# Kernel tuning notes

Measured on AMD Instinct MI355X. Metric: run time of the kernel, lower is better.

## Reference

```python
import jax, jax.numpy as jnp
import numpy as np

N_NODES = 10000
IN_DIM = 128
H1 = 32
H2 = 16
N_EDGES = 640000


def gcn_conv(x, W, b, row, col, n):
    """PyG-style GCNConv: add self-loops, symmetric deg^{-1/2} norm, linear, scatter-add."""
    loop = jnp.arange(n, dtype=row.dtype)
    r = jnp.concatenate([row, loop])
    c = jnp.concatenate([col, loop])
    deg = jax.ops.segment_sum(jnp.ones(r.shape[0], dtype=x.dtype), c, num_segments=n)
    dinv = jnp.where(deg > 0, jax.lax.rsqrt(deg), 0.0)
    norm = dinv[r] * dinv[c]                      # (E+N,)
    h = x @ W                                     # (N, out)
    msg = h[r] * norm[:, None]                    # gather + scale
    out = jax.ops.segment_sum(msg, c, num_segments=n)  # scatter-add
    return out + b


def setup_inputs() -> dict:
    key = jax.random.key(0)
    k1, k2, k3, k4, k5, k6 = jax.random.split(key, 6)
    x = jax.random.normal(k1, (N_NODES, IN_DIM), dtype=jnp.float32)
    edge_index = jax.random.randint(k2, (2, N_EDGES), 0, N_NODES, dtype=jnp.int64)
    # glorot-ish init for weights, zeros for bias (PyG defaults)
    W1 = jax.random.normal(k3, (IN_DIM, H1), dtype=jnp.float32) / np.sqrt(IN_DIM)
    b1 = jnp.zeros((H1,), dtype=jnp.float32)
    W2 = jax.random.normal(k4, (H1, H2), dtype=jnp.float32) / np.sqrt(H1)
    b2 = jnp.zeros((H2,), dtype=jnp.float32)
    return {"x": x, "edge_index": edge_index, "W1": W1, "b1": b1, "W2": W2, "b2": b2}


def reference(x, edge_index, W1, b1, W2, b2):
    row, col = edge_index[0], edge_index[1]
    n = x.shape[0]
    h = jax.nn.relu(gcn_conv(x, W1, b1, row, col, n))  # (N, H1)
    z = gcn_conv(h, W2, b2, row, col, n)               # (N, H2)
    logits = z @ z.T                                   # (N, N) dot-product decode
    return logits
```

## Files before the change

### kernel.cpp

```cpp
#include <hip/hip_runtime.h>

#define IN_DIM 128
#define H1 32
#define H2 16
#define PAD 160

#define XNODES 8
__global__ void k_fill_mm1(const int* __restrict__ row, const int* __restrict__ col,
                           int* __restrict__ deg, int* __restrict__ csrpad, int E,
                           const float* __restrict__ x, const float* __restrict__ W1,
                           float* __restrict__ hout, int N, int fillBlocks) {
    __shared__ float Ws[IN_DIM * H1];
    __shared__ float xs[XNODES][IN_DIM];
    if ((int)blockIdx.x < fillBlocks) {
        int e = blockIdx.x * blockDim.x + threadIdx.x;
        if (e < E) {
            int c = col[e];
            int pos = atomicAdd(&deg[c], 1);
            csrpad[(long)c * PAD + pos] = row[e];
        }
        return;
    }
    int t = threadIdx.x;
    int i0 = ((int)blockIdx.x - fillBlocks) * XNODES;
    const float4* W4 = reinterpret_cast<const float4*>(W1);
    float4* Ws4 = reinterpret_cast<float4*>(Ws);
#pragma unroll
    for (int i = t; i < IN_DIM * H1 / 4; i += 256) Ws4[i] = W4[i];
    const float4* xg = reinterpret_cast<const float4*>(x + (long)i0 * IN_DIM);
    float4* xs4 = reinterpret_cast<float4*>(xs);
    xs4[t] = xg[t];
    __syncthreads();
    int n = t >> 5, d = t & 31;
    float acc = 0.f;
#pragma unroll 8
    for (int k = 0; k < IN_DIM; ++k) acc = fmaf(xs[n][k], Ws[k * H1 + d], acc);
    int i = i0 + n;
    if (i < N) hout[(long)i * H1 + d] = acc;
}

__global__ void k_prep(const int* __restrict__ deg, float* __restrict__ dinv,
                       float* __restrict__ h, int N) {
    int i = blockIdx.x * blockDim.x + threadIdx.x;
    if (i >= N) return;
    float di = rsqrtf((float)deg[i] + 1.0f);
    dinv[i] = di;
    float4* hp = reinterpret_cast<float4*>(h + (long)i * H1);
#pragma unroll
    for (int q = 0; q < H1 / 4; ++q) {
        float4 v = hp[q];
        v.x *= di; v.y *= di; v.z *= di; v.w *= di;
        hp[q] = v;
    }
}

__global__ void k_g1mm2(const int* __restrict__ deg, const int* __restrict__ csrpad,
                        const float* __restrict__ dinv, const float* __restrict__ hp,
                        const float* __restrict__ b1, const float* __restrict__ W2,
                        float* __restrict__ h2p, int N) {
    __shared__ float W2s[H1 * H2];
    __shared__ float h1s[4][H1];
    int t = threadIdx.x;
    for (int i = t; i < H1 * H2; i += blockDim.x) W2s[i] = W2[i];
    __syncthreads();
    int wv = t >> 6;
    int lane = t & 63;
    int c = blockIdx.x * 4 + wv;
    bool active = (c < N);
    int cc = active ? c : (N - 1);
    constexpr int C4 = H1 / 4;
    constexpr int SUB = 64 / C4;
    int sub = lane / C4, d4 = lane % C4;
    int cnt = deg[cc];
    const int* bin = csrpad + (long)cc * PAD;
    const float4* hp4 = reinterpret_cast<const float4*>(hp);

    float4 A0 = make_float4(0.f, 0.f, 0.f, 0.f), A1 = A0, A2 = A0, A3 = A0;
    int k = sub;
    for (; k + 3 * SUB < cnt; k += 4 * SUB) {
        int s0 = bin[k];
        int s1 = bin[k + SUB];
        int s2 = bin[k + 2 * SUB];
        int s3 = bin[k + 3 * SUB];
        float4 v0 = hp4[(long)s0 * C4 + d4];
        float4 v1 = hp4[(long)s1 * C4 + d4];
        float4 v2 = hp4[(long)s2 * C4 + d4];
        float4 v3 = hp4[(long)s3 * C4 + d4];
        A0.x += v0.x; A0.y += v0.y; A0.z += v0.z; A0.w += v0.w;
        A1.x += v1.x; A1.y += v1.y; A1.z += v1.z; A1.w += v1.w;
        A2.x += v2.x; A2.y += v2.y; A2.z += v2.z; A2.w += v2.w;
        A3.x += v3.x; A3.y += v3.y; A3.z += v3.z; A3.w += v3.w;
    }
    for (; k < cnt; k += SUB) {
        float4 v = hp4[(long)bin[k] * C4 + d4];
        A0.x += v.x; A0.y += v.y; A0.z += v.z; A0.w += v.w;
    }
    float4 acc;
    acc.x = (A0.x + A1.x) + (A2.x + A3.x);
    acc.y = (A0.y + A1.y) + (A2.y + A3.y);
    acc.z = (A0.z + A1.z) + (A2.z + A3.z);
    acc.w = (A0.w + A1.w) + (A2.w + A3.w);
#pragma unroll
    for (int off = C4; off < 64; off <<= 1) {
        acc.x += __shfl_xor(acc.x, off, 64);
        acc.y += __shfl_xor(acc.y, off, 64);
        acc.z += __shfl_xor(acc.z, off, 64);
        acc.w += __shfl_xor(acc.w, off, 64);
    }
    if (lane < C4) {
        float di = dinv[cc];
        float4 self = hp4[(long)cc * C4 + d4];
        float4 bv = reinterpret_cast<const float4*>(b1)[d4];
        float4 v;
        v.x = fmaxf(fmaf(di, acc.x + self.x, bv.x), 0.f);
        v.y = fmaxf(fmaf(di, acc.y + self.y, bv.y), 0.f);
        v.z = fmaxf(fmaf(di, acc.z + self.z, bv.z), 0.f);
        v.w = fmaxf(fmaf(di, acc.w + self.w, bv.w), 0.f);
        reinterpret_cast<float4*>(h1s[wv])[d4] = v;
    }
    __syncthreads();
    if (active && lane < H2) {
        float z = 0.f;
#pragma unroll
        for (int kk = 0; kk < H1; ++kk) z = fmaf(h1s[wv][kk], W2s[kk * H2 + lane], z);
        h2p[(long)c * H2 + lane] = z * dinv[c];
    }
}

template <int D, bool RELU>
__global__ void k_gather(const int* __restrict__ deg, const int* __restrict__ csrpad,
                         const float* __restrict__ dinv, const float* __restrict__ hp,
                         const float* __restrict__ bias, float* __restrict__ out, int N) {
    constexpr int C4  = D / 4;
    constexpr int SUB = 64 / C4;
    int c = blockIdx.x * (blockDim.x >> 6) + (threadIdx.x >> 6);
    if (c >= N) return;
    int lane = threadIdx.x & 63;
    int sub = lane / C4, d4 = lane % C4;
    int cnt = deg[c];
    const int* bin = csrpad + (long)c * PAD;
    const float4* hp4 = reinterpret_cast<const float4*>(hp);

    float4 A0 = make_float4(0.f, 0.f, 0.f, 0.f), A1 = A0, A2 = A0, A3 = A0;
    int k = sub;
    for (; k + 3 * SUB < cnt; k += 4 * SUB) {
        int s0 = bin[k];
        int s1 = bin[k + SUB];
        int s2 = bin[k + 2 * SUB];
        int s3 = bin[k + 3 * SUB];
        float4 v0 = hp4[(long)s0 * C4 + d4];
        float4 v1 = hp4[(long)s1 * C4 + d4];
        float4 v2 = hp4[(long)s2 * C4 + d4];
        float4 v3 = hp4[(long)s3 * C4 + d4];
        A0.x += v0.x; A0.y += v0.y; A0.z += v0.z; A0.w += v0.w;
        A1.x += v1.x; A1.y += v1.y; A1.z += v1.z; A1.w += v1.w;
        A2.x += v2.x; A2.y += v2.y; A2.z += v2.z; A2.w += v2.w;
        A3.x += v3.x; A3.y += v3.y; A3.z += v3.z; A3.w += v3.w;
    }
    for (; k < cnt; k += SUB) {
        float4 v = hp4[(long)bin[k] * C4 + d4];
        A0.x += v.x; A0.y += v.y; A0.z += v.z; A0.w += v.w;
    }
    float4 acc;
    acc.x = (A0.x + A1.x) + (A2.x + A3.x);
    acc.y = (A0.y + A1.y) + (A2.y + A3.y);
    acc.z = (A0.z + A1.z) + (A2.z + A3.z);
    acc.w = (A0.w + A1.w) + (A2.w + A3.w);
#pragma unroll
    for (int off = C4; off < 64; off <<= 1) {
        acc.x += __shfl_xor(acc.x, off, 64);
        acc.y += __shfl_xor(acc.y, off, 64);
        acc.z += __shfl_xor(acc.z, off, 64);
        acc.w += __shfl_xor(acc.w, off, 64);
    }
    if (lane < C4) {
        float di = dinv[c];
        float4 self = hp4[(long)c * C4 + d4];
        float4 bv = reinterpret_cast<const float4*>(bias)[d4];
        float4 v;
        v.x = fmaf(di, acc.x + self.x, bv.x);
        v.y = fmaf(di, acc.y + self.y, bv.y);
        v.z = fmaf(di, acc.z + self.z, bv.z);
        v.w = fmaf(di, acc.w + self.w, bv.w);
        if (RELU) {
            v.x = fmaxf(v.x, 0.f); v.y = fmaxf(v.y, 0.f);
            v.z = fmaxf(v.z, 0.f); v.w = fmaxf(v.w, 0.f);
        }
        reinterpret_cast<float4*>(out + (long)c * D)[d4] = v;
    }
}


__global__ void k_count(const int* __restrict__ col, int* __restrict__ deg, int E) {
    int e = blockIdx.x * blockDim.x + threadIdx.x;
    if (e < E) atomicAdd(&deg[col[e]], 1);
}

template <int KD, int OD, bool SCALE>
__global__ void k_mm(const float* __restrict__ xin, const float* __restrict__ W,
                     const float* __restrict__ dinv, float* __restrict__ hout, int N) {
    __shared__ float Ws[KD * OD];
    for (int t = threadIdx.x; t < KD * OD; t += blockDim.x) Ws[t] = W[t];
    __syncthreads();
    int idx = blockIdx.x * blockDim.x + threadIdx.x;
    int i = idx / OD, d = idx % OD;
    if (i >= N) return;
    const float4* xr = reinterpret_cast<const float4*>(xin + (long)i * KD);
    float acc = 0.f;
#pragma unroll
    for (int k4 = 0; k4 < KD / 4; ++k4) {
        float4 xv = xr[k4];
        acc = fmaf(xv.x, Ws[(4 * k4 + 0) * OD + d], acc);
        acc = fmaf(xv.y, Ws[(4 * k4 + 1) * OD + d], acc);
        acc = fmaf(xv.z, Ws[(4 * k4 + 2) * OD + d], acc);
        acc = fmaf(xv.w, Ws[(4 * k4 + 3) * OD + d], acc);
    }
    hout[idx] = SCALE ? acc * dinv[i] : acc;
}

__global__ void k_dinv_i(const int* __restrict__ deg, float* __restrict__ dinv, int N) {
    int i = blockIdx.x * blockDim.x + threadIdx.x;
    if (i < N) dinv[i] = rsqrtf((float)deg[i] + 1.0f);
}

template <int D>
__global__ void k_scatter(const int* __restrict__ row, const int* __restrict__ col,
                          const float* __restrict__ dinv, const float* __restrict__ hin,
                          float* __restrict__ agg, int E) {
    int idx = blockIdx.x * blockDim.x + threadIdx.x;
    int e = idx / D, d = idx % D;
    if (e >= E) return;
    int r = row[e], c = col[e];
    float nrm = dinv[r] * dinv[c];
    atomicAdd(&agg[(long)c * D + d], hin[(long)r * D + d] * nrm);
}

template <int D, bool RELU>
__global__ void k_finish(const float* __restrict__ hproj, const float* __restrict__ dinv,
                         const float* __restrict__ bias, float* __restrict__ agg, int N) {
    int idx = blockIdx.x * blockDim.x + threadIdx.x;
    if (idx >= N * D) return;
    int i = idx / D, d = idx % D;
    float di = dinv[i];
    float v = agg[idx] + hproj[idx] * di * di + bias[d];
    agg[idx] = RELU ? fmaxf(v, 0.f) : v;
}

#define DT 128

__global__ __launch_bounds__(512, 8)
void k_decode(const float* __restrict__ z, float* __restrict__ out, int N) {
    __shared__ float ziT[16][DT];
    __shared__ float zjT[16][DT];
    int bi = blockIdx.y * DT, bj = blockIdx.x * DT;
    int t = threadIdx.x;

    {
        int r = (t >> 1) & 127;
        int gi = (t < 256 ? bi : bj) + r;
        int half = t & 1;
        float4 v0 = make_float4(0.f, 0.f, 0.f, 0.f), v1 = v0;
        if (gi < N) {
            const float4* zp = reinterpret_cast<const float4*>(z + (long)gi * 16);
            v0 = zp[half * 2];
            v1 = zp[half * 2 + 1];
        }
        float vals[8] = {v0.x, v0.y, v0.z, v0.w, v1.x, v1.y, v1.z, v1.w};
        float (*dst)[DT] = (t < 256) ? ziT : zjT;
        int k0 = half * 8;
#pragma unroll
        for (int k = 0; k < 8; ++k) dst[k0 + k][r] = vals[k];
    }
    __syncthreads();

    int tx = t & 15, ty = t >> 4;
    float acc[4][8] = {};
#pragma unroll 4
    for (int k = 0; k < 16; ++k) {
        float a[4], b[8];
        float4 a0 = *reinterpret_cast<const float4*>(&ziT[k][ty * 4]);
        float4 b0 = *reinterpret_cast<const float4*>(&zjT[k][tx * 4]);
        float4 b1 = *reinterpret_cast<const float4*>(&zjT[k][64 + tx * 4]);
        a[0]=a0.x; a[1]=a0.y; a[2]=a0.z; a[3]=a0.w;
        b[0]=b0.x; b[1]=b0.y; b[2]=b0.z; b[3]=b0.w;
        b[4]=b1.x; b[5]=b1.y; b[6]=b1.z; b[7]=b1.w;
#pragma unroll
        for (int u = 0; u < 4; ++u)
#pragma unroll
            for (int v = 0; v < 8; ++v)
                acc[u][v] = fmaf(a[u], b[v], acc[u][v]);
    }

#pragma unroll
    for (int u = 0; u < 4; ++u) {
        int gi = bi + ty * 4 + u;
        if (gi >= N) continue;
        int gj0 = bj + tx * 4;
        int gj1 = bj + 64 + tx * 4;
        long rowb = (long)gi * N;
        if (gj0 + 3 < N) {
            *reinterpret_cast<float4*>(&out[rowb + gj0]) =
                make_float4(acc[u][0], acc[u][1], acc[u][2], acc[u][3]);
        } else {
            for (int v2 = 0; v2 < 4; ++v2)
                if (gj0 + v2 < N) out[rowb + gj0 + v2] = acc[u][v2];
        }
        if (gj1 + 3 < N) {
            *reinterpret_cast<float4*>(&out[rowb + gj1]) =
                make_float4(acc[u][4], acc[u][5], acc[u][6], acc[u][7]);
        } else {
            for (int v2 = 0; v2 < 4; ++v2)
                if (gj1 + v2 < N) out[rowb + gj1 + v2] = acc[u][4 + v2];
        }
    }
}


extern "C" void kernel_launch(void* const* d_in, const int* in_sizes, int n_in,
                              void* d_out, int out_size, void* d_ws, size_t ws_size,
                              hipStream_t stream) {
    const float* x  = (const float*)d_in[0];
    const int*   ei = (const int*)d_in[1];
    const float* W1 = (const float*)d_in[2];
    const float* b1 = (const float*)d_in[3];
    const float* W2 = (const float*)d_in[4];
    const float* b2 = (const float*)d_in[5];
    float* out = (float*)d_out;

    const int N = in_sizes[0] / IN_DIM;
    const int E = in_sizes[1] / 2;
    const int* row = ei;
    const int* col = ei + E;

    const long SZ_DEG = (N + 15) & ~15L;
    const long SZ_BIN = (long)N * PAD;
    const long SZ_DI  = SZ_DEG;
    const long need = SZ_DEG + SZ_BIN + SZ_DI
                    + (long)N * H1 + 2L * N * H2;

    if (ws_size >= (size_t)need * 4) {
        int*   deg    = (int*)d_ws;
        int*   csrpad = deg + SZ_DEG;
        float* dinv   = (float*)(csrpad + SZ_BIN);
        float* h      = dinv + SZ_DI;
        float* h2p    = h + (long)N * H1;
        float* zz     = h2p + (long)N * H2;

        hipMemsetAsync(deg, 0, (size_t)N * sizeof(int), stream);

        int fillBlocks = (E + 255) / 256;
        int mmBlocks   = (N + XNODES - 1) / XNODES;
        k_fill_mm1<<<fillBlocks + mmBlocks, 256, 0, stream>>>(
            row, col, deg, csrpad, E, x, W1, h, N, fillBlocks);

        k_prep<<<(N + 255) / 256, 256, 0, stream>>>(deg, dinv, h, N);

        k_g1mm2<<<(N + 3) / 4, 256, 0, stream>>>(deg, csrpad, dinv, h, b1, W2, h2p, N);
        k_gather<H2, false><<<(N + 3) / 4, 256, 0, stream>>>(deg, csrpad, dinv, h2p, b2, zz, N);

        dim3 dgrid((N + DT - 1) / DT, (N + DT - 1) / DT);
        k_decode<<<dgrid, 512, 0, stream>>>(zz, out, N);
    } else {
        int*   deg  = (int*)d_ws;
        float* dinv = (float*)(deg + SZ_DEG);
        float* h    = dinv + SZ_DI;
        float* h1   = h + (long)N * H1;
        float* h2   = h1 + (long)N * H1;
        float* zz   = h2 + (long)N * H2;

        hipMemsetAsync(deg, 0, (size_t)N * sizeof(int), stream);
        hipMemsetAsync(h1, 0, (size_t)N * H1 * sizeof(float), stream);
        hipMemsetAsync(zz, 0, (size_t)N * H2 * sizeof(float), stream);

        k_count<<<(E + 255) / 256, 256, 0, stream>>>(col, deg, E);
        k_dinv_i<<<(N + 255) / 256, 256, 0, stream>>>(deg, dinv, N);

        k_mm<IN_DIM, H1, false><<<((long)N * H1 + 255) / 256, 256, 0, stream>>>(x, W1, dinv, h, N);
        k_scatter<H1><<<((long)E * H1 + 255) / 256, 256, 0, stream>>>(row, col, dinv, h, h1, E);
        k_finish<H1, true><<<((long)N * H1 + 255) / 256, 256, 0, stream>>>(h, dinv, b1, h1, N);

        k_mm<H1, H2, false><<<((long)N * H2 + 255) / 256, 256, 0, stream>>>(h1, W2, dinv, h2, N);
        k_scatter<H2><<<((long)E * H2 + 255) / 256, 256, 0, stream>>>(row, col, dinv, h2, zz, E);
        k_finish<H2, false><<<((long)N * H2 + 255) / 256, 256, 0, stream>>>(h2, dinv, b2, zz, N);

        dim3 dgrid((N + DT - 1) / DT, (N + DT - 1) / DT);
        k_decode<<<dgrid, 512, 0, stream>>>(zz, out, N);
    }
}
```

Before: 170.5 us.

## Fuse GCN pre-decode stages into one cooperative persistent kernel with grid syncs

Replaces the memset and the four pre-decode kernels (fill+mm1, prep, gather+mm2, gather) with one cooperative kernel of 512 persistent blocks. The stages are separated by grid.sync() calls. The aim is to remove per-kernel launch and drain overhead in the small-graph GCN stages. The cost is grid-wide barriers and lower parallelism per stage, since only 512 blocks run. The non-cooperative fallback path is also removed.

```diff
diff --git a/kernel.cpp b/kernel.cpp
--- a/kernel.cpp
+++ b/kernel.cpp
@@ -1,11 +1,201 @@
 #include <hip/hip_runtime.h>
+#include <hip/hip_cooperative_groups.h>
+namespace cg = cooperative_groups;
 
 #define IN_DIM 128
 #define H1 32
 #define H2 16
 #define PAD 160
-
 #define XNODES 8
+#define MGRID 512
+
+__global__ __launch_bounds__(256, 4) void k_mega(
+    const int* __restrict__ row, const int* __restrict__ col,
+    int* __restrict__ deg, int* __restrict__ csrpad,
+    const float* __restrict__ x, const float* __restrict__ W1,
+    const float* __restrict__ b1, const float* __restrict__ W2,
+    const float* __restrict__ b2, float* __restrict__ dinv,
+    float* __restrict__ h, float* __restrict__ h2p, float* __restrict__ zz,
+    int N, int E) {
+    cg::grid_group grid = cg::this_grid();
+    __shared__ float Ws[IN_DIM * H1];
+    __shared__ float xs[XNODES][IN_DIM];
+    __shared__ float h1s[4][H1];
+    int t = threadIdx.x;
+    int nth = (int)(gridDim.x * blockDim.x);
+    int gtid = (int)(blockIdx.x * blockDim.x) + t;
+
+    for (int i = gtid; i < N; i += nth) deg[i] = 0;
+    grid.sync();
+
+    for (int e = gtid; e < E; e += nth) {
+        int c = col[e];
+        int pos = atomicAdd(&deg[c], 1);
+        csrpad[(long)c * PAD + pos] = row[e];
+    }
+    {
+        const float4* W4 = reinterpret_cast<const float4*>(W1);
+        float4* Ws4 = reinterpret_cast<float4*>(Ws);
+        for (int i = t; i < IN_DIM * H1 / 4; i += 256) Ws4[i] = W4[i];
+    }
+    int ngroups = (N + XNODES - 1) / XNODES;
+    for (int g = (int)blockIdx.x; g < ngroups; g += (int)gridDim.x) {
+        __syncthreads();
+        int i0 = g * XNODES;
+        int gi = i0 + (t >> 5);
+        float4 xv = make_float4(0.f, 0.f, 0.f, 0.f);
+        if (gi < N) xv = reinterpret_cast<const float4*>(x)[(long)i0 * 32 + t];
+        reinterpret_cast<float4*>(xs)[t] = xv;
+        __syncthreads();
+        int n = t >> 5, d = t & 31;
+        float acc = 0.f;
+#pragma unroll 8
+        for (int k = 0; k < IN_DIM; ++k) acc = fmaf(xs[n][k], Ws[k * H1 + d], acc);
+        int i = i0 + n;
+        if (i < N) h[(long)i * H1 + d] = acc;
+    }
+    grid.sync();
+
+    for (int i = gtid; i < N; i += nth) {
+        float di = rsqrtf((float)deg[i] + 1.0f);
+        dinv[i] = di;
+        float4* hp = reinterpret_cast<float4*>(h + (long)i * H1);
+#pragma unroll
+        for (int q = 0; q < H1 / 4; ++q) {
+            float4 v = hp[q];
+            v.x *= di; v.y *= di; v.z *= di; v.w *= di;
+            hp[q] = v;
+        }
+    }
+    grid.sync();
+
+    for (int i = t; i < H1 * H2; i += 256) Ws[i] = W2[i];
+    __syncthreads();
+    int wv = t >> 6, lane = t & 63;
+    {
+        constexpr int C4 = H1 / 4;
+        constexpr int SUB = 64 / C4;
+        int sub = lane / C4, d4 = lane % C4;
+        const float4* hp4 = reinterpret_cast<const float4*>(h);
+        for (int c0 = (int)blockIdx.x * 4; c0 < N; c0 += (int)gridDim.x * 4) {
+            int c = c0 + wv;
+            bool active = (c < N);
+            int cc = active ? c : (N - 1);
+            int cnt = deg[cc];
+            const int* bin = csrpad + (long)cc * PAD;
+            float4 A0 = make_float4(0.f, 0.f, 0.f, 0.f), A1 = A0, A2 = A0, A3 = A0;
+            int k = sub;
+            for (; k + 3 * SUB < cnt; k += 4 * SUB) {
+                int s0 = bin[k];
+                int s1 = bin[k + SUB];
+                int s2 = bin[k + 2 * SUB];
+                int s3 = bin[k + 3 * SUB];
+                float4 v0 = hp4[(long)s0 * C4 + d4];
+                float4 v1 = hp4[(long)s1 * C4 + d4];
+                float4 v2 = hp4[(long)s2 * C4 + d4];
+                float4 v3 = hp4[(long)s3 * C4 + d4];
+                A0.x += v0.x; A0.y += v0.y; A0.z += v0.z; A0.w += v0.w;
+                A1.x += v1.x; A1.y += v1.y; A1.z += v1.z; A1.w += v1.w;
+                A2.x += v2.x; A2.y += v2.y; A2.z += v2.z; A2.w += v2.w;
+                A3.x += v3.x; A3.y += v3.y; A3.z += v3.z; A3.w += v3.w;
+            }
+            for (; k < cnt; k += SUB) {
+                float4 v = hp4[(long)bin[k] * C4 + d4];
+                A0.x += v.x; A0.y += v.y; A0.z += v.z; A0.w += v.w;
+            }
+            float4 acc;
+            acc.x = (A0.x + A1.x) + (A2.x + A3.x);
+            acc.y = (A0.y + A1.y) + (A2.y + A3.y);
+            acc.z = (A0.z + A1.z) + (A2.z + A3.z);
+            acc.w = (A0.w + A1.w) + (A2.w + A3.w);
+#pragma unroll
+            for (int off = C4; off < 64; off <<= 1) {
+                acc.x += __shfl_xor(acc.x, off, 64);
+                acc.y += __shfl_xor(acc.y, off, 64);
+                acc.z += __shfl_xor(acc.z, off, 64);
+                acc.w += __shfl_xor(acc.w, off, 64);
+            }
+            __syncthreads();
+            if (lane < C4) {
+                float di = dinv[cc];
+                float4 self = hp4[(long)cc * C4 + d4];
+                float4 bv = reinterpret_cast<const float4*>(b1)[d4];
+                float4 v;
+                v.x = fmaxf(fmaf(di, acc.x + self.x, bv.x), 0.f);
+                v.y = fmaxf(fmaf(di, acc.y + self.y, bv.y), 0.f);
+                v.z = fmaxf(fmaf(di, acc.z + self.z, bv.z), 0.f);
+                v.w = fmaxf(fmaf(di, acc.w + self.w, bv.w), 0.f);
+                reinterpret_cast<float4*>(h1s[wv])[d4] = v;
+            }
+            __syncthreads();
+            if (active && lane < H2) {
+                float z = 0.f;
+#pragma unroll
+                for (int kk = 0; kk < H1; ++kk) z = fmaf(h1s[wv][kk], Ws[kk * H2 + lane], z);
+                h2p[(long)c * H2 + lane] = z * dinv[c];
+            }
+        }
+    }
+    grid.sync();
+
+    {
+        constexpr int C4 = H2 / 4;
+        constexpr int SUB = 64 / C4;
+        int sub = lane / C4, d4 = lane % C4;
+        const float4* hp4 = reinterpret_cast<const float4*>(h2p);
+        for (int c0 = (int)blockIdx.x * 4; c0 < N; c0 += (int)gridDim.x * 4) {
+            int c = c0 + wv;
+            if (c >= N) continue;
+            int cnt = deg[c];
+            const int* bin = csrpad + (long)c * PAD;
+            float4 A0 = make_float4(0.f, 0.f, 0.f, 0.f), A1 = A0, A2 = A0, A3 = A0;
+            int k = sub;
+            for (; k + 3 * SUB < cnt; k += 4 * SUB) {
+                int s0 = bin[k];
+                int s1 = bin[k + SUB];
+                int s2 = bin[k + 2 * SUB];
+                int s3 = bin[k + 3 * SUB];
+                float4 v0 = hp4[(long)s0 * C4 + d4];
+                float4 v1 = hp4[(long)s1 * C4 + d4];
+                float4 v2 = hp4[(long)s2 * C4 + d4];
+                float4 v3 = hp4[(long)s3 * C4 + d4];
+                A0.x += v0.x; A0.y += v0.y; A0.z += v0.z; A0.w += v0.w;
+                A1.x += v1.x; A1.y += v1.y; A1.z += v1.z; A1.w += v1.w;
+                A2.x += v2.x; A2.y += v2.y; A2.z += v2.z; A2.w += v2.w;
+                A3.x += v3.x; A3.y += v3.y; A3.z += v3.z; A3.w += v3.w;
+            }
+            for (; k < cnt; k += SUB) {
+                float4 v = hp4[(long)bin[k] * C4 + d4];
+                A0.x += v.x; A0.y += v.y; A0.z += v.z; A0.w += v.w;
+            }
+            float4 acc;
+            acc.x = (A0.x + A1.x) + (A2.x + A3.x);
+            acc.y = (A0.y + A1.y) + (A2.y + A3.y);
+            acc.z = (A0.z + A1.z) + (A2.z + A3.z);
+            acc.w = (A0.w + A1.w) + (A2.w + A3.w);
+#pragma unroll
+            for (int off = C4; off < 64; off <<= 1) {
+                acc.x += __shfl_xor(acc.x, off, 64);
+                acc.y += __shfl_xor(acc.y, off, 64);
+                acc.z += __shfl_xor(acc.z, off, 64);
+                acc.w += __shfl_xor(acc.w, off, 64);
+            }
+            if (lane < C4) {
+                float di = dinv[c];
+                float4 self = hp4[(long)c * C4 + d4];
+                float4 bv = reinterpret_cast<const float4*>(b2)[d4];
+                float4 v;
+                v.x = fmaf(di, acc.x + self.x, bv.x);
+                v.y = fmaf(di, acc.y + self.y, bv.y);
+                v.z = fmaf(di, acc.z + self.z, bv.z);
+                v.w = fmaf(di, acc.w + self.w, bv.w);
+                reinterpret_cast<float4*>(zz + (long)c * H2)[d4] = v;
+            }
+        }
+    }
+}
+
+
 __global__ void k_fill_mm1(const int* __restrict__ row, const int* __restrict__ col,
                            int* __restrict__ deg, int* __restrict__ csrpad, int E,
                            const float* __restrict__ x, const float* __restrict__ W1,
@@ -190,62 +380,6 @@
     }
 }
 
-
-__global__ void k_count(const int* __restrict__ col, int* __restrict__ deg, int E) {
-    int e = blockIdx.x * blockDim.x + threadIdx.x;
-    if (e < E) atomicAdd(&deg[col[e]], 1);
-}
-
-template <int KD, int OD, bool SCALE>
-__global__ void k_mm(const float* __restrict__ xin, const float* __restrict__ W,
-                     const float* __restrict__ dinv, float* __restrict__ hout, int N) {
-    __shared__ float Ws[KD * OD];
-    for (int t = threadIdx.x; t < KD * OD; t += blockDim.x) Ws[t] = W[t];
-    __syncthreads();
-    int idx = blockIdx.x * blockDim.x + threadIdx.x;
-    int i = idx / OD, d = idx % OD;
-    if (i >= N) return;
-    const float4* xr = reinterpret_cast<const float4*>(xin + (long)i * KD);
-    float acc = 0.f;
-#pragma unroll
-    for (int k4 = 0; k4 < KD / 4; ++k4) {
-        float4 xv = xr[k4];
-        acc = fmaf(xv.x, Ws[(4 * k4 + 0) * OD + d], acc);
-        acc = fmaf(xv.y, Ws[(4 * k4 + 1) * OD + d], acc);
-        acc = fmaf(xv.z, Ws[(4 * k4 + 2) * OD + d], acc);
-        acc = fmaf(xv.w, Ws[(4 * k4 + 3) * OD + d], acc);
-    }
-    hout[idx] = SCALE ? acc * dinv[i] : acc;
-}
-
-__global__ void k_dinv_i(const int* __restrict__ deg, float* __restrict__ dinv, int N) {
-    int i = blockIdx.x * blockDim.x + threadIdx.x;
-    if (i < N) dinv[i] = rsqrtf((float)deg[i] + 1.0f);
-}
-
-template <int D>
-__global__ void k_scatter(const int* __restrict__ row, const int* __restrict__ col,
-                          const float* __restrict__ dinv, const float* __restrict__ hin,
-                          float* __restrict__ agg, int E) {
-    int idx = blockIdx.x * blockDim.x + threadIdx.x;
-    int e = idx / D, d = idx % D;
-    if (e >= E) return;
-    int r = row[e], c = col[e];
-    float nrm = dinv[r] * dinv[c];
-    atomicAdd(&agg[(long)c * D + d], hin[(long)r * D + d] * nrm);
-}
-
-template <int D, bool RELU>
-__global__ void k_finish(const float* __restrict__ hproj, const float* __restrict__ dinv,
-                         const float* __restrict__ bias, float* __restrict__ agg, int N) {
-    int idx = blockIdx.x * blockDim.x + threadIdx.x;
-    if (idx >= N * D) return;
-    int i = idx / D, d = idx % D;
-    float di = dinv[i];
-    float v = agg[idx] + hproj[idx] * di * di + bias[d];
-    agg[idx] = RELU ? fmaxf(v, 0.f) : v;
-}
-
 #define DT 128
 
 __global__ __launch_bounds__(512, 8)
@@ -335,55 +469,31 @@
     const long SZ_DEG = (N + 15) & ~15L;
     const long SZ_BIN = (long)N * PAD;
     const long SZ_DI  = SZ_DEG;
-    const long need = SZ_DEG + SZ_BIN + SZ_DI
-                    + (long)N * H1 + 2L * N * H2;
-
-    if (ws_size >= (size_t)need * 4) {
-        int*   deg    = (int*)d_ws;
-        int*   csrpad = deg + SZ_DEG;
-        float* dinv   = (float*)(csrpad + SZ_BIN);
-        float* h      = dinv + SZ_DI;
-        float* h2p    = h + (long)N * H1;
-        float* zz     = h2p + (long)N * H2;
-
+
+    int*   deg    = (int*)d_ws;
+    int*   csrpad = deg + SZ_DEG;
+    float* dinv   = (float*)(csrpad + SZ_BIN);
+    float* h      = dinv + SZ_DI;
+    float* h2p    = h + (long)N * H1;
+    float* zz     = h2p + (long)N * H2;
+
+    void* args[] = {(void*)&row, (void*)&col, (void*)&deg, (void*)&csrpad,
+                    (void*)&x, (void*)&W1, (void*)&b1, (void*)&W2, (void*)&b2,
+                    (void*)&dinv, (void*)&h, (void*)&h2p, (void*)&zz,
+                    (void*)&N, (void*)&E};
+    hipError_t ce = hipLaunchCooperativeKernel((void*)k_mega, dim3(MGRID), dim3(256),
+                                               args, 0, stream);
+    if (ce != hipSuccess) {
         hipMemsetAsync(deg, 0, (size_t)N * sizeof(int), stream);
-
         int fillBlocks = (E + 255) / 256;
         int mmBlocks   = (N + XNODES - 1) / XNODES;
         k_fill_mm1<<<fillBlocks + mmBlocks, 256, 0, stream>>>(
             row, col, deg, csrpad, E, x, W1, h, N, fillBlocks);
-
         k_prep<<<(N + 255) / 256, 256, 0, stream>>>(deg, dinv, h, N);
-
         k_g1mm2<<<(N + 3) / 4, 256, 0, stream>>>(deg, csrpad, dinv, h, b1, W2, h2p, N);
         k_gather<H2, false><<<(N + 3) / 4, 256, 0, stream>>>(deg, csrpad, dinv, h2p, b2, zz, N);
-
-        dim3 dgrid((N + DT - 1) / DT, (N + DT - 1) / DT);
-        k_decode<<<dgrid, 512, 0, stream>>>(zz, out, N);
-    } else {
-        int*   deg  = (int*)d_ws;
-        float* dinv = (float*)(deg + SZ_DEG);
-        float* h    = dinv + SZ_DI;
-        float* h1   = h + (long)N * H1;
-        float* h2   = h1 + (long)N * H1;
-        float* zz   = h2 + (long)N * H2;
-
-        hipMemsetAsync(deg, 0, (size_t)N * sizeof(int), stream);
-        hipMemsetAsync(h1, 0, (size_t)N * H1 * sizeof(float), stream);
-        hipMemsetAsync(zz, 0, (size_t)N * H2 * sizeof(float), stream);
-
-        k_count<<<(E + 255) / 256, 256, 0, stream>>>(col, deg, E);
-        k_dinv_i<<<(N + 255) / 256, 256, 0, stream>>>(deg, dinv, N);
-
-        k_mm<IN_DIM, H1, false><<<((long)N * H1 + 255) / 256, 256, 0, stream>>>(x, W1, dinv, h, N);
-        k_scatter<H1><<<((long)E * H1 + 255) / 256, 256, 0, stream>>>(row, col, dinv, h, h1, E);
-        k_finish<H1, true><<<((long)N * H1 + 255) / 256, 256, 0, stream>>>(h, dinv, b1, h1, N);
-
-        k_mm<H1, H2, false><<<((long)N * H2 + 255) / 256, 256, 0, stream>>>(h1, W2, dinv, h2, N);
-        k_scatter<H2><<<((long)E * H2 + 255) / 256, 256, 0, stream>>>(row, col, dinv, h2, zz, E);
-        k_finish<H2, false><<<((long)N * H2 + 255) / 256, 256, 0, stream>>>(h2, dinv, b2, zz, N);
-
-        dim3 dgrid((N + DT - 1) / DT, (N + DT - 1) / DT);
-        k_decode<<<dgrid, 512, 0, stream>>>(zz, out, N);
-    }
-}
+    }
+
+    dim3 dgrid((N + DT - 1) / DT, (N + DT - 1) / DT);
+    k_decode<<<dgrid, 512, 0, stream>>>(zz, out, N);
+}
```

New measurement: 387.0 us. 2.27x slower.
